# Optimization experiments

Measured on AMD Instinct MI355X. Metric: run time of the kernel, lower is better.

## Reference

```python
import jax, jax.numpy as jnp
import numpy as np

N = 100000
E = 1600000
IN_C, HID_C, OUT_C = 128, 64, 64
NEG_SLOPE = 0.2


def setup_inputs() -> dict:
    key = jax.random.key(0)
    ks = jax.random.split(key, 12)
    x = jax.random.normal(ks[0], (N, IN_C), dtype=jnp.float32)
    edge_index = jax.random.randint(ks[1], (2, E), 0, N, dtype=jnp.int64)
    s = 0.1
    # layer 1: heads=2, out=HID_C, concat=True
    W1 = jax.random.normal(ks[2], (IN_C, 2 * HID_C), dtype=jnp.float32) * s
    a_src1 = jax.random.normal(ks[3], (2, HID_C), dtype=jnp.float32) * s
    a_dst1 = jax.random.normal(ks[4], (2, HID_C), dtype=jnp.float32) * s
    b1 = jnp.zeros((2 * HID_C,), dtype=jnp.float32)
    # layer 2: heads=1, out=OUT_C, concat=False
    W2 = jax.random.normal(ks[5], (2 * HID_C, OUT_C), dtype=jnp.float32) * s
    a_src2 = jax.random.normal(ks[6], (1, OUT_C), dtype=jnp.float32) * s
    a_dst2 = jax.random.normal(ks[7], (1, OUT_C), dtype=jnp.float32) * s
    b2 = jnp.zeros((OUT_C,), dtype=jnp.float32)
    return {"x": x, "edge_index": edge_index, "W1": W1, "a_src1": a_src1,
            "a_dst1": a_dst1, "b1": b1, "W2": W2, "a_src2": a_src2,
            "a_dst2": a_dst2, "b2": b2}


def gat_conv(x, src, dst, W, a_src, a_dst, bias, heads, out_ch, concat):
    n = x.shape[0]
    h = (x @ W).reshape(n, heads, out_ch)            # [N,H,C]
    alpha_s = jnp.einsum('nhc,hc->nh', h, a_src)     # [N,H]
    alpha_d = jnp.einsum('nhc,hc->nh', h, a_dst)
    e = jax.nn.leaky_relu(alpha_s[src] + alpha_d[dst], NEG_SLOPE)  # [E,H]
    emax = jax.ops.segment_max(e, dst, num_segments=n)
    e = jnp.exp(e - emax[dst])
    denom = jax.ops.segment_sum(e, dst, num_segments=n)
    alpha = e / (denom[dst] + 1e-16)                 # edge softmax over dst
    out = jax.ops.segment_sum(h[src] * alpha[:, :, None], dst, num_segments=n)
    out = out.reshape(n, heads * out_ch) if concat else out.mean(axis=1)
    return out + bias


def reference(x, edge_index, W1, a_src1, a_dst1, b1, W2, a_src2, a_dst2, b2):
    # PyG GATConv adds self-loops by default; append once (same graph both layers)
    loop = jnp.arange(N, dtype=edge_index.dtype)
    src = jnp.concatenate([edge_index[0], loop])
    dst = jnp.concatenate([edge_index[1], loop])
    h = jax.nn.elu(gat_conv(x, src, dst, W1, a_src1, a_dst1, b1, 2, HID_C, True))
    out = jax.nn.elu(gat_conv(h, src, dst, W2, a_src2, a_dst2, b2, 1, OUT_C, False))
    return out
```

## Files before the change

### kernel.cpp

```cpp
#include <hip/hip_runtime.h>
#include <hip/hip_bf16.h>
#include <math.h>

#define N_NODES 100000
#define N_EDGES 1600000
#define TOT_E   (N_EDGES + N_NODES)

__device__ __forceinline__ float lrelu(float v){ return v > 0.f ? v : 0.2f * v; }
__device__ __forceinline__ float elu_(float v){ return v > 0.f ? v : expm1f(v); }
__device__ __forceinline__ ushort f2bf(float f){
  unsigned u = __float_as_uint(f);
  u = (u + 0x7FFFu + ((u >> 16) & 1u)) >> 16;
  return (ushort)u;
}
__device__ __forceinline__ float bf2f(ushort u){
  return __uint_as_float(((unsigned)u) << 16);
}
__device__ __forceinline__ float bflo(unsigned p){ return __uint_as_float(p << 16); }
__device__ __forceinline__ float bfhi(unsigned p){ return __uint_as_float(p & 0xffff0000u); }

__global__ __launch_bounds__(256) void k_count(const int* __restrict__ ei, int* __restrict__ cnt){
  int i = blockIdx.x * 256 + threadIdx.x;
  if (i >= TOT_E) return;
  int d = (i < N_EDGES) ? ei[N_EDGES + i] : (i - N_EDGES);
  atomicAdd(&cnt[d], 1);
}

__global__ __launch_bounds__(1024) void k_scan1(const int* __restrict__ cnt, int* __restrict__ off,
                                                int* __restrict__ bs){
  __shared__ int s[1024];
  int t = threadIdx.x;
  int i = blockIdx.x * 1024 + t;
  int v = (i < N_NODES) ? cnt[i] : 0;
  s[t] = v;
  __syncthreads();
  for (int o = 1; o < 1024; o <<= 1){
    int tmp = 0;
    if (t >= o) tmp = s[t - o];
    __syncthreads();
    if (t >= o) s[t] += tmp;
    __syncthreads();
  }
  if (i < N_NODES) off[i] = s[t] - v;
  if (t == 1023) bs[blockIdx.x] = s[1023];
}

__global__ __launch_bounds__(128) void k_scan2(int* __restrict__ bs, int* __restrict__ off, int nb){
  __shared__ int s[128];
  int t = threadIdx.x;
  int v = (t < nb) ? bs[t] : 0;
  s[t] = v;
  __syncthreads();
  #pragma unroll
  for (int o = 1; o < 128; o <<= 1){
    int tmp = 0;
    if (t >= o) tmp = s[t - o];
    __syncthreads();
    if (t >= o) s[t] += tmp;
    __syncthreads();
  }
  if (t < nb) bs[t] = s[t] - v;
  if (t == nb - 1) off[N_NODES] = s[t];
}

__global__ __launch_bounds__(1024) void k_scan3(int* __restrict__ off, int* __restrict__ cur,
                                                const int* __restrict__ bs){
  int i = blockIdx.x * 1024 + threadIdx.x;
  if (i < N_NODES){
    int v = off[i] + bs[blockIdx.x];
    off[i] = v;
    cur[i] = v;
  }
}

__global__ __launch_bounds__(256) void k_fill_w(const int* __restrict__ ei, int* __restrict__ cur,
                                                uint4* __restrict__ csr4,
                                                const float* __restrict__ as1, const float* __restrict__ ad1){
  int i = blockIdx.x * 256 + threadIdx.x;
  if (i >= TOT_E) return;
  int s, d;
  if (i < N_EDGES){ s = ei[i]; d = ei[N_EDGES + i]; }
  else            { s = d = i - N_EDGES; }
  int p = atomicAdd(&cur[d], 1);
  float2 a  = *(const float2*)(as1 + 2u * (unsigned)s);
  float2 ad = *(const float2*)(ad1 + 2u * (unsigned)d);
  uint4 v;
  v.x = (unsigned)s;
  v.y = __float_as_uint(__expf(lrelu(a.x + ad.x)));
  v.z = __float_as_uint(__expf(lrelu(a.y + ad.y)));
  v.w = (unsigned)d;
  csr4[p] = v;
}

__global__ __launch_bounds__(256) void k_ew2(const uint4* __restrict__ csr4,
                                             const float* __restrict__ as2, const float* __restrict__ ad2,
                                             uint2* __restrict__ ew){
  int i = blockIdx.x * 256 + threadIdx.x;
  if (i >= TOT_E) return;
  uint4 v = csr4[i];
  float w = __expf(lrelu(as2[v.x] + ad2[v.w]));
  ew[i] = make_uint2(v.x, __float_as_uint(w));
}

__global__ __launch_bounds__(256) void k_gemm1(const float* __restrict__ x, const float* __restrict__ W,
                                               const float* __restrict__ a_src, const float* __restrict__ a_dst,
                                               ushort* __restrict__ h, float* __restrict__ as1,
                                               float* __restrict__ ad1, int n){
  __shared__ float sx[128][36];
  __shared__ float sw[32][132];
  const int tid  = threadIdx.x;
  const int cg   = tid & 7;
  const int slot = tid >> 3;
  const int rbase = blockIdx.x * 128;
  const int r0   = rbase + slot * 4;
  const int col0 = cg * 16;

  float acc[4][16] = {};

  for (int kc = 0; kc < 4; ++kc){
    __syncthreads();
    #pragma unroll
    for (int i = 0; i < 4; ++i){
      int f   = tid + 256 * i;
      int row = f >> 3;
      int c4  = f & 7;
      int gr  = rbase + row; if (gr > n - 1) gr = n - 1;
      float4 v = *(const float4*)(x + (size_t)gr * 128 + kc * 32 + c4 * 4);
      *(float4*)(&sx[row][c4 * 4]) = v;
    }
    #pragma unroll
    for (int i = 0; i < 4; ++i){
      int f  = tid + 256 * i;
      int k  = f >> 5;
      int c4 = f & 31;
      float4 v = *(const float4*)(W + (size_t)(kc * 32 + k) * 128 + c4 * 4);
      *(float4*)(&sw[k][c4 * 4]) = v;
    }
    __syncthreads();

    #pragma unroll 8
    for (int j = 0; j < 32; ++j){
      float4 w0 = *(const float4*)(&sw[j][col0]);
      float4 w1 = *(const float4*)(&sw[j][col0 + 4]);
      float4 w2 = *(const float4*)(&sw[j][col0 + 8]);
      float4 w3 = *(const float4*)(&sw[j][col0 + 12]);
      #pragma unroll
      for (int i = 0; i < 4; ++i){
        float xv = sx[slot * 4 + i][j];
        acc[i][0]  = fmaf(xv, w0.x, acc[i][0]);  acc[i][1]  = fmaf(xv, w0.y, acc[i][1]);
        acc[i][2]  = fmaf(xv, w0.z, acc[i][2]);  acc[i][3]  = fmaf(xv, w0.w, acc[i][3]);
        acc[i][4]  = fmaf(xv, w1.x, acc[i][4]);  acc[i][5]  = fmaf(xv, w1.y, acc[i][5]);
        acc[i][6]  = fmaf(xv, w1.z, acc[i][6]);  acc[i][7]  = fmaf(xv, w1.w, acc[i][7]);
        acc[i][8]  = fmaf(xv, w2.x, acc[i][8]);  acc[i][9]  = fmaf(xv, w2.y, acc[i][9]);
        acc[i][10] = fmaf(xv, w2.z, acc[i][10]); acc[i][11] = fmaf(xv, w2.w, acc[i][11]);
        acc[i][12] = fmaf(xv, w3.x, acc[i][12]); acc[i][13] = fmaf(xv, w3.y, acc[i][13]);
        acc[i][14] = fmaf(xv, w3.z, acc[i][14]); acc[i][15] = fmaf(xv, w3.w, acc[i][15]);
      }
    }
  }

  #pragma unroll
  for (int i = 0; i < 4; ++i){
    int r = r0 + i;
    float sp = 0.f, dp = 0.f;
    #pragma unroll
    for (int j = 0; j < 16; ++j){
      sp = fmaf(acc[i][j], a_src[col0 + j], sp);
      dp = fmaf(acc[i][j], a_dst[col0 + j], dp);
    }
    float s0 = (col0 < 64) ? sp : 0.f, s1 = (col0 < 64) ? 0.f : sp;
    float d0 = (col0 < 64) ? dp : 0.f, d1 = (col0 < 64) ? 0.f : dp;
    #pragma unroll
    for (int m = 1; m <= 4; m <<= 1){
      s0 += __shfl_xor(s0, m); s1 += __shfl_xor(s1, m);
      d0 += __shfl_xor(d0, m); d1 += __shfl_xor(d1, m);
    }
    if (r < n){
      union { uint4 q[2]; ushort us[16]; } pk;
      #pragma unroll
      for (int j = 0; j < 16; ++j) pk.us[j] = f2bf(acc[i][j]);
      uint4* dst = (uint4*)(h + (size_t)r * 128 + col0);
      dst[0] = pk.q[0]; dst[1] = pk.q[1];
      if (cg == 0){
        as1[2 * r] = s0; as1[2 * r + 1] = s1;
        ad1[2 * r] = d0; ad1[2 * r + 1] = d1;
      }
    }
  }
}

__global__ void k_prep2(const float* __restrict__ W2, const float* __restrict__ a_src2,
                        const float* __restrict__ a_dst2, float* __restrict__ vs, float* __restrict__ vd){
  int k = threadIdx.x;
  float s = 0.f, d = 0.f;
  for (int c = 0; c < 64; ++c){
    float w = W2[k * 64 + c];
    s = fmaf(w, a_src2[c], s);
    d = fmaf(w, a_dst2[c], d);
  }
  vs[k] = s; vd[k] = d;
}

__global__ __launch_bounds__(256) void k_agg1(const int* __restrict__ off, const uint4* __restrict__ csr4,
                                              const ushort* __restrict__ h,
                                              const float* __restrict__ b,
                                              const float* __restrict__ vs2, const float* __restrict__ vd2,
                                              const float* __restrict__ W2,
                                              ushort* __restrict__ z, float* __restrict__ as2,
                                              float* __restrict__ ad2){
  __shared__ float yly[4][128];
  int wid  = threadIdx.x >> 6;
  int node = blockIdx.x * 4 + wid;
  int lane = threadIdx.x & 63;
  int head = lane >> 5;
  int c0   = lane * 2;
  int s0 = off[node], e0 = off[node + 1];

  float acc0 = 0.f, acc1 = 0.f, den = 0.f;
  int k = s0;
  for (; k + 7 < e0; k += 8){
    int ku = __builtin_amdgcn_readfirstlane(k);
    uint4 eA = csr4[ku],     eB = csr4[ku + 1], eC = csr4[ku + 2], eD = csr4[ku + 3];
    uint4 eE = csr4[ku + 4], eF = csr4[ku + 5], eG = csr4[ku + 6], eH = csr4[ku + 7];
    unsigned hA = *(const unsigned*)(h + ((size_t)eA.x << 7) + c0);
    unsigned hB = *(const unsigned*)(h + ((size_t)eB.x << 7) + c0);
    unsigned hC = *(const unsigned*)(h + ((size_t)eC.x << 7) + c0);
    unsigned hD = *(const unsigned*)(h + ((size_t)eD.x << 7) + c0);
    unsigned hE = *(const unsigned*)(h + ((size_t)eE.x << 7) + c0);
    unsigned hF = *(const unsigned*)(h + ((size_t)eF.x << 7) + c0);
    unsigned hG = *(const unsigned*)(h + ((size_t)eG.x << 7) + c0);
    unsigned hH = *(const unsigned*)(h + ((size_t)eH.x << 7) + c0);
    float wA = __uint_as_float(head ? eA.z : eA.y);
    float wB = __uint_as_float(head ? eB.z : eB.y);
    float wC = __uint_as_float(head ? eC.z : eC.y);
    float wD = __uint_as_float(head ? eD.z : eD.y);
    float wE = __uint_as_float(head ? eE.z : eE.y);
    float wF = __uint_as_float(head ? eF.z : eF.y);
    float wG = __uint_as_float(head ? eG.z : eG.y);
    float wH = __uint_as_float(head ? eH.z : eH.y);
    den += ((wA + wB) + (wC + wD)) + ((wE + wF) + (wG + wH));
    acc0 = fmaf(wA, bflo(hA), acc0); acc1 = fmaf(wA, bfhi(hA), acc1);
    acc0 = fmaf(wB, bflo(hB), acc0); acc1 = fmaf(wB, bfhi(hB), acc1);
    acc0 = fmaf(wC, bflo(hC), acc0); acc1 = fmaf(wC, bfhi(hC), acc1);
    acc0 = fmaf(wD, bflo(hD), acc0); acc1 = fmaf(wD, bfhi(hD), acc1);
    acc0 = fmaf(wE, bflo(hE), acc0); acc1 = fmaf(wE, bfhi(hE), acc1);
    acc0 = fmaf(wF, bflo(hF), acc0); acc1 = fmaf(wF, bfhi(hF), acc1);
    acc0 = fmaf(wG, bflo(hG), acc0); acc1 = fmaf(wG, bfhi(hG), acc1);
    acc0 = fmaf(wH, bflo(hH), acc0); acc1 = fmaf(wH, bfhi(hH), acc1);
  }
  for (; k < e0; ++k){
    int ku = __builtin_amdgcn_readfirstlane(k);
    uint4 eA = csr4[ku];
    unsigned hA = *(const unsigned*)(h + ((size_t)eA.x << 7) + c0);
    float wA = __uint_as_float(head ? eA.z : eA.y);
    den += wA;
    acc0 = fmaf(wA, bflo(hA), acc0); acc1 = fmaf(wA, bfhi(hA), acc1);
  }

  float inv = 1.f / (den + 1e-16f);
  float o0 = elu_(acc0 * inv + b[c0]);
  float o1 = elu_(acc1 * inv + b[c0 + 1]);

  *(float2*)(&yly[wid][c0]) = make_float2(o0, o1);

  float s2 = fmaf(o0, vs2[c0], o1 * vs2[c0 + 1]);
  float d2 = fmaf(o0, vd2[c0], o1 * vd2[c0 + 1]);
  #pragma unroll
  for (int m = 32; m; m >>= 1){ s2 += __shfl_xor(s2, m); d2 += __shfl_xor(d2, m); }
  if (lane == 0){ as2[node] = s2; ad2[node] = d2; }

  asm volatile("s_waitcnt lgkmcnt(0)" ::: "memory");

  float zacc = 0.f;
  const float* yw = yly[wid];
  #pragma unroll 4
  for (int q = 0; q < 32; ++q){
    float4 yv = *(const float4*)(yw + 4 * q);
    const float* wr = W2 + (q * 4) * 64 + lane;
    zacc = fmaf(yv.x, wr[0],   zacc);
    zacc = fmaf(yv.y, wr[64],  zacc);
    zacc = fmaf(yv.z, wr[128], zacc);
    zacc = fmaf(yv.w, wr[192], zacc);
  }
  z[((unsigned)node << 6) + lane] = f2bf(zacc);
}

__global__ __launch_bounds__(256) void k_agg2(const int* __restrict__ off, const uint2* __restrict__ ew,
                                              const ushort* __restrict__ z,
                                              const float* __restrict__ b2, float* __restrict__ out){
  int node = blockIdx.x * 4 + (threadIdx.x >> 6);
  int lane = threadIdx.x & 63;
  int s0 = off[node], e0 = off[node + 1];

  float acc = 0.f, den = 0.f;
  int k = s0;
  for (; k + 7 < e0; k += 8){
    int ku = __builtin_amdgcn_readfirstlane(k);
    uint2 eA = ew[ku],     eB = ew[ku + 1], eC = ew[ku + 2], eD = ew[ku + 3];
    uint2 eE = ew[ku + 4], eF = ew[ku + 5], eG = ew[ku + 6], eH = ew[ku + 7];
    ushort zA = z[((size_t)eA.x << 6) + lane];
    ushort zB = z[((size_t)eB.x << 6) + lane];
    ushort zC = z[((size_t)eC.x << 6) + lane];
    ushort zD = z[((size_t)eD.x << 6) + lane];
    ushort zE = z[((size_t)eE.x << 6) + lane];
    ushort zF = z[((size_t)eF.x << 6) + lane];
    ushort zG = z[((size_t)eG.x << 6) + lane];
    ushort zH = z[((size_t)eH.x << 6) + lane];
    float wA = __uint_as_float(eA.y), wB = __uint_as_float(eB.y);
    float wC = __uint_as_float(eC.y), wD = __uint_as_float(eD.y);
    float wE = __uint_as_float(eE.y), wF = __uint_as_float(eF.y);
    float wG = __uint_as_float(eG.y), wH = __uint_as_float(eH.y);
    den += ((wA + wB) + (wC + wD)) + ((wE + wF) + (wG + wH));
    acc = fmaf(wA, bf2f(zA), acc); acc = fmaf(wB, bf2f(zB), acc);
    acc = fmaf(wC, bf2f(zC), acc); acc = fmaf(wD, bf2f(zD), acc);
    acc = fmaf(wE, bf2f(zE), acc); acc = fmaf(wF, bf2f(zF), acc);
    acc = fmaf(wG, bf2f(zG), acc); acc = fmaf(wH, bf2f(zH), acc);
  }
  for (; k < e0; ++k){
    int ku = __builtin_amdgcn_readfirstlane(k);
    uint2 eA = ew[ku];
    ushort zA = z[((size_t)eA.x << 6) + lane];
    float wA = __uint_as_float(eA.y);
    den += wA;
    acc = fmaf(wA, bf2f(zA), acc);
  }

  float inv = 1.f / (den + 1e-16f);
  out[((unsigned)node << 6) + lane] = elu_(acc * inv + b2[lane]);
}

extern "C" void kernel_launch(void* const* d_in, const int* in_sizes, int n_in,
                              void* d_out, int out_size, void* d_ws, size_t ws_size,
                              hipStream_t stream){
  const float* x      = (const float*)d_in[0];
  const int*   ei     = (const int*)d_in[1];
  const float* W1     = (const float*)d_in[2];
  const float* a_src1 = (const float*)d_in[3];
  const float* a_dst1 = (const float*)d_in[4];
  const float* b1     = (const float*)d_in[5];
  const float* W2     = (const float*)d_in[6];
  const float* a_src2 = (const float*)d_in[7];
  const float* a_dst2 = (const float*)d_in[8];
  const float* b2     = (const float*)d_in[9];
  float* out = (float*)d_out;

  char* ws = (char*)d_ws;
  size_t o = 0;
  auto alloc = [&](size_t bytes){ size_t r = o; o = (o + bytes + 255) & ~(size_t)255; return r; };
  int*    tmpN = (int*)(ws + alloc((size_t)N_NODES * 4));
  int*    bs   = (int*)(ws + alloc(512));
  int*    off  = (int*)(ws + alloc((size_t)(N_NODES + 1) * 4));
  uint4*  csr4 = (uint4*)(ws + alloc((size_t)TOT_E * 16));
  uint2*  ew   = (uint2*)(ws + alloc((size_t)TOT_E * 8));
  float*  as1  = (float*)(ws + alloc((size_t)N_NODES * 2 * 4));
  float*  ad1  = (float*)(ws + alloc((size_t)N_NODES * 2 * 4));
  float*  as2  = (float*)(ws + alloc((size_t)N_NODES * 4));
  float*  ad2  = (float*)(ws + alloc((size_t)N_NODES * 4));
  float*  vs2  = (float*)(ws + alloc(512));
  float*  vd2  = (float*)(ws + alloc(512));
  ushort* z    = (ushort*)(ws + alloc((size_t)N_NODES * 64 * 2));
  ushort* h1   = (ushort*)d_out;
  (void)ws_size; (void)in_sizes; (void)n_in; (void)out_size;

  const int nblk_edges = (TOT_E + 255) / 256;
  const int nblk_scan  = (N_NODES + 1023) / 1024;
  const int nblk_wave4 = N_NODES / 4;

  k_gemm1<<<(N_NODES + 127) / 128, 256, 0, stream>>>(x, W1, a_src1, a_dst1, h1, as1, ad1, N_NODES);
  k_prep2<<<1, 128, 0, stream>>>(W2, a_src2, a_dst2, vs2, vd2);

  hipMemsetAsync(tmpN, 0, (size_t)N_NODES * 4, stream);
  k_count <<<nblk_edges, 256, 0, stream>>>(ei, tmpN);
  k_scan1 <<<nblk_scan, 1024, 0, stream>>>(tmpN, off, bs);
  k_scan2 <<<1, 128, 0, stream>>>(bs, off, nblk_scan);
  k_scan3 <<<nblk_scan, 1024, 0, stream>>>(off, tmpN, bs);
  k_fill_w<<<nblk_edges, 256, 0, stream>>>(ei, tmpN, csr4, as1, ad1);

  k_agg1 <<<nblk_wave4, 256, 0, stream>>>(off, csr4, h1, b1, vs2, vd2, W2, z, as2, ad2);

  k_ew2  <<<nblk_edges, 256, 0, stream>>>(csr4, as2, ad2, ew);
  k_agg2 <<<nblk_wave4, 256, 0, stream>>>(off, ew, z, b2, out);
}
```

Measured before the change: 409.2 us.

## Fuse layer-2 edge weight computation into aggregation and add 4-edge tail step

Removes the separate k_ew2 pass that computed layer-2 softmax numerators into a packed edge array. k_agg2 now reads csr4 directly and computes exp(lrelu(as2[src]+ad2[dst])) inline, with the destination term loaded once per node. This saves one kernel launch and a full edge-array write and read. In exchange, k_agg2 reads 16-byte edge records instead of 8-byte ones and does extra gathers and exp calls, repeated across all 64 lanes. Both aggregation kernels also gain a 4-edge unrolled step before the scalar tail loop.

```diff
diff --git a/kernel.cpp b/kernel.cpp
--- a/kernel.cpp
+++ b/kernel.cpp
@@ -90,16 +90,6 @@
   v.z = __float_as_uint(__expf(lrelu(a.y + ad.y)));
   v.w = (unsigned)d;
   csr4[p] = v;
-}
-
-__global__ __launch_bounds__(256) void k_ew2(const uint4* __restrict__ csr4,
-                                             const float* __restrict__ as2, const float* __restrict__ ad2,
-                                             uint2* __restrict__ ew){
-  int i = blockIdx.x * 256 + threadIdx.x;
-  if (i >= TOT_E) return;
-  uint4 v = csr4[i];
-  float w = __expf(lrelu(as2[v.x] + ad2[v.w]));
-  ew[i] = make_uint2(v.x, __float_as_uint(w));
 }
 
 __global__ __launch_bounds__(256) void k_gemm1(const float* __restrict__ x, const float* __restrict__ W,
@@ -248,6 +238,24 @@
     acc0 = fmaf(wG, bflo(hG), acc0); acc1 = fmaf(wG, bfhi(hG), acc1);
     acc0 = fmaf(wH, bflo(hH), acc0); acc1 = fmaf(wH, bfhi(hH), acc1);
   }
+  if (k + 3 < e0){
+    int ku = __builtin_amdgcn_readfirstlane(k);
+    uint4 eA = csr4[ku],     eB = csr4[ku + 1], eC = csr4[ku + 2], eD = csr4[ku + 3];
+    unsigned hA = *(const unsigned*)(h + ((size_t)eA.x << 7) + c0);
+    unsigned hB = *(const unsigned*)(h + ((size_t)eB.x << 7) + c0);
+    unsigned hC = *(const unsigned*)(h + ((size_t)eC.x << 7) + c0);
+    unsigned hD = *(const unsigned*)(h + ((size_t)eD.x << 7) + c0);
+    float wA = __uint_as_float(head ? eA.z : eA.y);
+    float wB = __uint_as_float(head ? eB.z : eB.y);
+    float wC = __uint_as_float(head ? eC.z : eC.y);
+    float wD = __uint_as_float(head ? eD.z : eD.y);
+    den += (wA + wB) + (wC + wD);
+    acc0 = fmaf(wA, bflo(hA), acc0); acc1 = fmaf(wA, bfhi(hA), acc1);
+    acc0 = fmaf(wB, bflo(hB), acc0); acc1 = fmaf(wB, bfhi(hB), acc1);
+    acc0 = fmaf(wC, bflo(hC), acc0); acc1 = fmaf(wC, bfhi(hC), acc1);
+    acc0 = fmaf(wD, bflo(hD), acc0); acc1 = fmaf(wD, bfhi(hD), acc1);
+    k += 4;
+  }
   for (; k < e0; ++k){
     int ku = __builtin_amdgcn_readfirstlane(k);
     uint4 eA = csr4[ku];
@@ -285,19 +293,21 @@
   z[((unsigned)node << 6) + lane] = f2bf(zacc);
 }
 
-__global__ __launch_bounds__(256) void k_agg2(const int* __restrict__ off, const uint2* __restrict__ ew,
-                                              const ushort* __restrict__ z,
+__global__ __launch_bounds__(256) void k_agg2(const int* __restrict__ off, const uint4* __restrict__ csr4,
+                                              const ushort* __restrict__ z, const float* __restrict__ as2,
+                                              const float* __restrict__ ad2,
                                               const float* __restrict__ b2, float* __restrict__ out){
   int node = blockIdx.x * 4 + (threadIdx.x >> 6);
   int lane = threadIdx.x & 63;
   int s0 = off[node], e0 = off[node + 1];
+  float adv = ad2[node];
 
   float acc = 0.f, den = 0.f;
   int k = s0;
   for (; k + 7 < e0; k += 8){
     int ku = __builtin_amdgcn_readfirstlane(k);
-    uint2 eA = ew[ku],     eB = ew[ku + 1], eC = ew[ku + 2], eD = ew[ku + 3];
-    uint2 eE = ew[ku + 4], eF = ew[ku + 5], eG = ew[ku + 6], eH = ew[ku + 7];
+    uint4 eA = csr4[ku],     eB = csr4[ku + 1], eC = csr4[ku + 2], eD = csr4[ku + 3];
+    uint4 eE = csr4[ku + 4], eF = csr4[ku + 5], eG = csr4[ku + 6], eH = csr4[ku + 7];
     ushort zA = z[((size_t)eA.x << 6) + lane];
     ushort zB = z[((size_t)eB.x << 6) + lane];
     ushort zC = z[((size_t)eC.x << 6) + lane];
@@ -306,21 +316,41 @@
     ushort zF = z[((size_t)eF.x << 6) + lane];
     ushort zG = z[((size_t)eG.x << 6) + lane];
     ushort zH = z[((size_t)eH.x << 6) + lane];
-    float wA = __uint_as_float(eA.y), wB = __uint_as_float(eB.y);
-    float wC = __uint_as_float(eC.y), wD = __uint_as_float(eD.y);
-    float wE = __uint_as_float(eE.y), wF = __uint_as_float(eF.y);
-    float wG = __uint_as_float(eG.y), wH = __uint_as_float(eH.y);
+    float wA = __expf(lrelu(as2[eA.x] + adv));
+    float wB = __expf(lrelu(as2[eB.x] + adv));
+    float wC = __expf(lrelu(as2[eC.x] + adv));
+    float wD = __expf(lrelu(as2[eD.x] + adv));
+    float wE = __expf(lrelu(as2[eE.x] + adv));
+    float wF = __expf(lrelu(as2[eF.x] + adv));
+    float wG = __expf(lrelu(as2[eG.x] + adv));
+    float wH = __expf(lrelu(as2[eH.x] + adv));
     den += ((wA + wB) + (wC + wD)) + ((wE + wF) + (wG + wH));
     acc = fmaf(wA, bf2f(zA), acc); acc = fmaf(wB, bf2f(zB), acc);
     acc = fmaf(wC, bf2f(zC), acc); acc = fmaf(wD, bf2f(zD), acc);
     acc = fmaf(wE, bf2f(zE), acc); acc = fmaf(wF, bf2f(zF), acc);
     acc = fmaf(wG, bf2f(zG), acc); acc = fmaf(wH, bf2f(zH), acc);
   }
+  if (k + 3 < e0){
+    int ku = __builtin_amdgcn_readfirstlane(k);
+    uint4 eA = csr4[ku], eB = csr4[ku + 1], eC = csr4[ku + 2], eD = csr4[ku + 3];
+    ushort zA = z[((size_t)eA.x << 6) + lane];
+    ushort zB = z[((size_t)eB.x << 6) + lane];
+    ushort zC = z[((size_t)eC.x << 6) + lane];
+    ushort zD = z[((size_t)eD.x << 6) + lane];
+    float wA = __expf(lrelu(as2[eA.x] + adv));
+    float wB = __expf(lrelu(as2[eB.x] + adv));
+    float wC = __expf(lrelu(as2[eC.x] + adv));
+    float wD = __expf(lrelu(as2[eD.x] + adv));
+    den += (wA + wB) + (wC + wD);
+    acc = fmaf(wA, bf2f(zA), acc); acc = fmaf(wB, bf2f(zB), acc);
+    acc = fmaf(wC, bf2f(zC), acc); acc = fmaf(wD, bf2f(zD), acc);
+    k += 4;
+  }
   for (; k < e0; ++k){
     int ku = __builtin_amdgcn_readfirstlane(k);
-    uint2 eA = ew[ku];
+    uint4 eA = csr4[ku];
     ushort zA = z[((size_t)eA.x << 6) + lane];
-    float wA = __uint_as_float(eA.y);
+    float wA = __expf(lrelu(as2[eA.x] + adv));
     den += wA;
     acc = fmaf(wA, bf2f(zA), acc);
   }
@@ -351,7 +381,6 @@
   int*    bs   = (int*)(ws + alloc(512));
   int*    off  = (int*)(ws + alloc((size_t)(N_NODES + 1) * 4));
   uint4*  csr4 = (uint4*)(ws + alloc((size_t)TOT_E * 16));
-  uint2*  ew   = (uint2*)(ws + alloc((size_t)TOT_E * 8));
   float*  as1  = (float*)(ws + alloc((size_t)N_NODES * 2 * 4));
   float*  ad1  = (float*)(ws + alloc((size_t)N_NODES * 2 * 4));
   float*  as2  = (float*)(ws + alloc((size_t)N_NODES * 4));
@@ -378,6 +407,5 @@
 
   k_agg1 <<<nblk_wave4, 256, 0, stream>>>(off, csr4, h1, b1, vs2, vd2, W2, z, as2, ad2);
 
-  k_ew2  <<<nblk_edges, 256, 0, stream>>>(csr4, as2, ad2, ew);
-  k_agg2 <<<nblk_wave4, 256, 0, stream>>>(off, ew, z, b2, out);
-}
+  k_agg2 <<<nblk_wave4, 256, 0, stream>>>(off, csr4, z, as2, ad2, b2, out);
+}
```

Result: no change. 411.5 us (+0.6%).

## Split CSR into index and weight arrays, fuse layer-2 edge weights into aggregation

Applied to the files above, without the earlier changes.

Replaces the 16-byte per-edge record with a 4-byte source-index array plus an 8-byte weight-pair array, and drops the separate k_ew2 kernel. k_agg2 now computes the layer-2 attention weights inline from as2/ad2 instead of reading a precomputed edge-weight array. Both aggregation kernels switch to batched 16/8/4/1 unrolled gathers with all index loads issued first. This cuts edge-array traffic and one launch, at the cost of an extra gather of as2 per edge, extra exp work inside agg2, and more registers.

```diff
diff --git a/kernel.cpp b/kernel.cpp
--- a/kernel.cpp
+++ b/kernel.cpp
@@ -74,7 +74,7 @@
 }
 
 __global__ __launch_bounds__(256) void k_fill_w(const int* __restrict__ ei, int* __restrict__ cur,
-                                                uint4* __restrict__ csr4,
+                                                unsigned* __restrict__ csre, float2* __restrict__ wpair,
                                                 const float* __restrict__ as1, const float* __restrict__ ad1){
   int i = blockIdx.x * 256 + threadIdx.x;
   if (i >= TOT_E) return;
@@ -84,22 +84,8 @@
   int p = atomicAdd(&cur[d], 1);
   float2 a  = *(const float2*)(as1 + 2u * (unsigned)s);
   float2 ad = *(const float2*)(ad1 + 2u * (unsigned)d);
-  uint4 v;
-  v.x = (unsigned)s;
-  v.y = __float_as_uint(__expf(lrelu(a.x + ad.x)));
-  v.z = __float_as_uint(__expf(lrelu(a.y + ad.y)));
-  v.w = (unsigned)d;
-  csr4[p] = v;
-}
-
-__global__ __launch_bounds__(256) void k_ew2(const uint4* __restrict__ csr4,
-                                             const float* __restrict__ as2, const float* __restrict__ ad2,
-                                             uint2* __restrict__ ew){
-  int i = blockIdx.x * 256 + threadIdx.x;
-  if (i >= TOT_E) return;
-  uint4 v = csr4[i];
-  float w = __expf(lrelu(as2[v.x] + ad2[v.w]));
-  ew[i] = make_uint2(v.x, __float_as_uint(w));
+  csre[p] = (unsigned)s;
+  wpair[p] = make_float2(__expf(lrelu(a.x + ad.x)), __expf(lrelu(a.y + ad.y)));
 }
 
 __global__ __launch_bounds__(256) void k_gemm1(const float* __restrict__ x, const float* __restrict__ W,
@@ -201,7 +187,32 @@
   vs[k] = s; vd[k] = d;
 }
 
-__global__ __launch_bounds__(256) void k_agg1(const int* __restrict__ off, const uint4* __restrict__ csr4,
+#define AGG1_BATCH(NB)                                                          \
+  {                                                                             \
+    int ku = __builtin_amdgcn_readfirstlane(k);                                 \
+    unsigned sidx[NB]; unsigned hv[NB]; float wv[NB];                           \
+    _Pragma("unroll")                                                           \
+    for (int j = 0; j < NB; ++j) sidx[j] = csre[ku + j];                        \
+    _Pragma("unroll")                                                           \
+    for (int j = 0; j < NB; ++j)                                                \
+      hv[j] = *(const unsigned*)(h + ((size_t)sidx[j] << 7) + c0);              \
+    _Pragma("unroll")                                                           \
+    for (int j = 0; j < NB; ++j){                                               \
+      float2 wp = wpair[ku + j];                                                \
+      wv[j] = head ? wp.y : wp.x;                                               \
+    }                                                                           \
+    _Pragma("unroll")                                                           \
+    for (int j = 0; j < NB; ++j){                                               \
+      den += wv[j];                                                             \
+      acc0 = fmaf(wv[j], bflo(hv[j]), acc0);                                    \
+      acc1 = fmaf(wv[j], bfhi(hv[j]), acc1);                                    \
+    }                                                                           \
+    k += NB;                                                                    \
+  }
+
+__global__ __launch_bounds__(256) void k_agg1(const int* __restrict__ off,
+                                              const unsigned* __restrict__ csre,
+                                              const float2* __restrict__ wpair,
                                               const ushort* __restrict__ h,
                                               const float* __restrict__ b,
                                               const float* __restrict__ vs2, const float* __restrict__ vd2,
@@ -218,43 +229,11 @@
 
   float acc0 = 0.f, acc1 = 0.f, den = 0.f;
   int k = s0;
-  for (; k + 7 < e0; k += 8){
-    int ku = __builtin_amdgcn_readfirstlane(k);
-    uint4 eA = csr4[ku],     eB = csr4[ku + 1], eC = csr4[ku + 2], eD = csr4[ku + 3];
-    uint4 eE = csr4[ku + 4], eF = csr4[ku + 5], eG = csr4[ku + 6], eH = csr4[ku + 7];
-    unsigned hA = *(const unsigned*)(h + ((size_t)eA.x << 7) + c0);
-    unsigned hB = *(const unsigned*)(h + ((size_t)eB.x << 7) + c0);
-    unsigned hC = *(const unsigned*)(h + ((size_t)eC.x << 7) + c0);
-    unsigned hD = *(const unsigned*)(h + ((size_t)eD.x << 7) + c0);
-    unsigned hE = *(const unsigned*)(h + ((size_t)eE.x << 7) + c0);
-    unsigned hF = *(const unsigned*)(h + ((size_t)eF.x << 7) + c0);
-    unsigned hG = *(const unsigned*)(h + ((size_t)eG.x << 7) + c0);
-    unsigned hH = *(const unsigned*)(h + ((size_t)eH.x << 7) + c0);
-    float wA = __uint_as_float(head ? eA.z : eA.y);
-    float wB = __uint_as_float(head ? eB.z : eB.y);
-    float wC = __uint_as_float(head ? eC.z : eC.y);
-    float wD = __uint_as_float(head ? eD.z : eD.y);
-    float wE = __uint_as_float(head ? eE.z : eE.y);
-    float wF = __uint_as_float(head ? eF.z : eF.y);
-    float wG = __uint_as_float(head ? eG.z : eG.y);
-    float wH = __uint_as_float(head ? eH.z : eH.y);
-    den += ((wA + wB) + (wC + wD)) + ((wE + wF) + (wG + wH));
-    acc0 = fmaf(wA, bflo(hA), acc0); acc1 = fmaf(wA, bfhi(hA), acc1);
-    acc0 = fmaf(wB, bflo(hB), acc0); acc1 = fmaf(wB, bfhi(hB), acc1);
-    acc0 = fmaf(wC, bflo(hC), acc0); acc1 = fmaf(wC, bfhi(hC), acc1);
-    acc0 = fmaf(wD, bflo(hD), acc0); acc1 = fmaf(wD, bfhi(hD), acc1);
-    acc0 = fmaf(wE, bflo(hE), acc0); acc1 = fmaf(wE, bfhi(hE), acc1);
-    acc0 = fmaf(wF, bflo(hF), acc0); acc1 = fmaf(wF, bfhi(hF), acc1);
-    acc0 = fmaf(wG, bflo(hG), acc0); acc1 = fmaf(wG, bfhi(hG), acc1);
-    acc0 = fmaf(wH, bflo(hH), acc0); acc1 = fmaf(wH, bfhi(hH), acc1);
-  }
-  for (; k < e0; ++k){
-    int ku = __builtin_amdgcn_readfirstlane(k);
-    uint4 eA = csr4[ku];
-    unsigned hA = *(const unsigned*)(h + ((size_t)eA.x << 7) + c0);
-    float wA = __uint_as_float(head ? eA.z : eA.y);
-    den += wA;
-    acc0 = fmaf(wA, bflo(hA), acc0); acc1 = fmaf(wA, bfhi(hA), acc1);
+  while (k + 15 < e0) AGG1_BATCH(16)
+  if (k + 7 < e0)  AGG1_BATCH(8)
+  if (k + 3 < e0)  AGG1_BATCH(4)
+  for (; k < e0; ){
+    AGG1_BATCH(1)
   }
 
   float inv = 1.f / (den + 1e-16f);
@@ -285,44 +264,43 @@
   z[((unsigned)node << 6) + lane] = f2bf(zacc);
 }
 
-__global__ __launch_bounds__(256) void k_agg2(const int* __restrict__ off, const uint2* __restrict__ ew,
-                                              const ushort* __restrict__ z,
+#define AGG2_BATCH(NB)                                                          \
+  {                                                                             \
+    int ku = __builtin_amdgcn_readfirstlane(k);                                 \
+    unsigned sidx[NB]; ushort zv[NB]; float wv[NB];                             \
+    _Pragma("unroll")                                                           \
+    for (int j = 0; j < NB; ++j) sidx[j] = csre[ku + j];                        \
+    _Pragma("unroll")                                                           \
+    for (int j = 0; j < NB; ++j)                                                \
+      zv[j] = z[((size_t)sidx[j] << 6) + lane];                                 \
+    _Pragma("unroll")                                                           \
+    for (int j = 0; j < NB; ++j)                                                \
+      wv[j] = __expf(lrelu(as2[sidx[j]] + adv));                                \
+    _Pragma("unroll")                                                           \
+    for (int j = 0; j < NB; ++j){                                               \
+      den += wv[j];                                                             \
+      acc = fmaf(wv[j], bf2f(zv[j]), acc);                                      \
+    }                                                                           \
+    k += NB;                                                                    \
+  }
+
+__global__ __launch_bounds__(256) void k_agg2(const int* __restrict__ off,
+                                              const unsigned* __restrict__ csre,
+                                              const ushort* __restrict__ z, const float* __restrict__ as2,
+                                              const float* __restrict__ ad2,
                                               const float* __restrict__ b2, float* __restrict__ out){
   int node = blockIdx.x * 4 + (threadIdx.x >> 6);
   int lane = threadIdx.x & 63;
   int s0 = off[node], e0 = off[node + 1];
+  float adv = ad2[node];
 
   float acc = 0.f, den = 0.f;
   int k = s0;
-  for (; k + 7 < e0; k += 8){
-    int ku = __builtin_amdgcn_readfirstlane(k);
-    uint2 eA = ew[ku],     eB = ew[ku + 1], eC = ew[ku + 2], eD = ew[ku + 3];
-    uint2 eE = ew[ku + 4], eF = ew[ku + 5], eG = ew[ku + 6], eH = ew[ku + 7];
-    ushort zA = z[((size_t)eA.x << 6) + lane];
-    ushort zB = z[((size_t)eB.x << 6) + lane];
-    ushort zC = z[((size_t)eC.x << 6) + lane];
-    ushort zD = z[((size_t)eD.x << 6) + lane];
-    ushort zE = z[((size_t)eE.x << 6) + lane];
-    ushort zF = z[((size_t)eF.x << 6) + lane];
-    ushort zG = z[((size_t)eG.x << 6) + lane];
-    ushort zH = z[((size_t)eH.x << 6) + lane];
-    float wA = __uint_as_float(eA.y), wB = __uint_as_float(eB.y);
-    float wC = __uint_as_float(eC.y), wD = __uint_as_float(eD.y);
-    float wE = __uint_as_float(eE.y), wF = __uint_as_float(eF.y);
-    float wG = __uint_as_float(eG.y), wH = __uint_as_float(eH.y);
-    den += ((wA + wB) + (wC + wD)) + ((wE + wF) + (wG + wH));
-    acc = fmaf(wA, bf2f(zA), acc); acc = fmaf(wB, bf2f(zB), acc);
-    acc = fmaf(wC, bf2f(zC), acc); acc = fmaf(wD, bf2f(zD), acc);
-    acc = fmaf(wE, bf2f(zE), acc); acc = fmaf(wF, bf2f(zF), acc);
-    acc = fmaf(wG, bf2f(zG), acc); acc = fmaf(wH, bf2f(zH), acc);
-  }
-  for (; k < e0; ++k){
-    int ku = __builtin_amdgcn_readfirstlane(k);
-    uint2 eA = ew[ku];
-    ushort zA = z[((size_t)eA.x << 6) + lane];
-    float wA = __uint_as_float(eA.y);
-    den += wA;
-    acc = fmaf(wA, bf2f(zA), acc);
+  while (k + 15 < e0) AGG2_BATCH(16)
+  if (k + 7 < e0)  AGG2_BATCH(8)
+  if (k + 3 < e0)  AGG2_BATCH(4)
+  for (; k < e0; ){
+    AGG2_BATCH(1)
   }
 
   float inv = 1.f / (den + 1e-16f);
@@ -347,19 +325,19 @@
   char* ws = (char*)d_ws;
   size_t o = 0;
   auto alloc = [&](size_t bytes){ size_t r = o; o = (o + bytes + 255) & ~(size_t)255; return r; };
-  int*    tmpN = (int*)(ws + alloc((size_t)N_NODES * 4));
-  int*    bs   = (int*)(ws + alloc(512));
-  int*    off  = (int*)(ws + alloc((size_t)(N_NODES + 1) * 4));
-  uint4*  csr4 = (uint4*)(ws + alloc((size_t)TOT_E * 16));
-  uint2*  ew   = (uint2*)(ws + alloc((size_t)TOT_E * 8));
-  float*  as1  = (float*)(ws + alloc((size_t)N_NODES * 2 * 4));
-  float*  ad1  = (float*)(ws + alloc((size_t)N_NODES * 2 * 4));
-  float*  as2  = (float*)(ws + alloc((size_t)N_NODES * 4));
-  float*  ad2  = (float*)(ws + alloc((size_t)N_NODES * 4));
-  float*  vs2  = (float*)(ws + alloc(512));
-  float*  vd2  = (float*)(ws + alloc(512));
-  ushort* z    = (ushort*)(ws + alloc((size_t)N_NODES * 64 * 2));
-  ushort* h1   = (ushort*)d_out;
+  int*      tmpN  = (int*)(ws + alloc((size_t)N_NODES * 4));
+  int*      bs    = (int*)(ws + alloc(512));
+  int*      off   = (int*)(ws + alloc((size_t)(N_NODES + 1) * 4));
+  unsigned* csre  = (unsigned*)(ws + alloc((size_t)TOT_E * 4));
+  float2*   wpair = (float2*)(ws + alloc((size_t)TOT_E * 8));
+  float*    as1   = (float*)(ws + alloc((size_t)N_NODES * 2 * 4));
+  float*    ad1   = (float*)(ws + alloc((size_t)N_NODES * 2 * 4));
+  float*    as2   = (float*)(ws + alloc((size_t)N_NODES * 4));
+  float*    ad2   = (float*)(ws + alloc((size_t)N_NODES * 4));
+  float*    vs2   = (float*)(ws + alloc(512));
+  float*    vd2   = (float*)(ws + alloc(512));
+  ushort*   z     = (ushort*)(ws + alloc((size_t)N_NODES * 64 * 2));
+  ushort*   h1    = (ushort*)d_out;
   (void)ws_size; (void)in_sizes; (void)n_in; (void)out_size;
 
   const int nblk_edges = (TOT_E + 255) / 256;
@@ -374,10 +352,9 @@
   k_scan1 <<<nblk_scan, 1024, 0, stream>>>(tmpN, off, bs);
   k_scan2 <<<1, 128, 0, stream>>>(bs, off, nblk_scan);
   k_scan3 <<<nblk_scan, 1024, 0, stream>>>(off, tmpN, bs);
-  k_fill_w<<<nblk_edges, 256, 0, stream>>>(ei, tmpN, csr4, as1, ad1);
-
-  k_agg1 <<<nblk_wave4, 256, 0, stream>>>(off, csr4, h1, b1, vs2, vd2, W2, z, as2, ad2);
-
-  k_ew2  <<<nblk_edges, 256, 0, stream>>>(csr4, as2, ad2, ew);
-  k_agg2 <<<nblk_wave4, 256, 0, stream>>>(off, ew, z, b2, out);
-}
+  k_fill_w<<<nblk_edges, 256, 0, stream>>>(ei, tmpN, csre, wpair, as1, ad1);
+
+  k_agg1 <<<nblk_wave4, 256, 0, stream>>>(off, csre, wpair, h1, b1, vs2, vd2, W2, z, as2, ad2);
+
+  k_agg2 <<<nblk_wave4, 256, 0, stream>>>(off, csre, z, as2, ad2, b2, out);
+}
```

New measurement: 413.6 us. Within noise of the previous version (+1.1%).
